# Kernel tuning notes

Measured on AMD Instinct MI355X. Metric: run time of the kernel, lower is better.

Reference implementation:

```python
import jax, jax.numpy as jnp
import numpy as np

N, E, DIN, DH, DOUT = 100000, 600000, 128, 128, 64


def _glorot(k, shape):
    lim = float(np.sqrt(6.0 / (shape[0] + shape[1])))
    return jax.random.uniform(k, shape, jnp.float32, -lim, lim)


def setup_inputs() -> dict:
    key = jax.random.key(0)
    ks = jax.random.split(key, 12)
    return {
        "x": jax.random.normal(ks[0], (N, DIN), jnp.float32),
        "src": jax.random.randint(ks[1], (E,), 0, N),
        "dst": jax.random.randint(ks[2], (E,), 0, N),
        # layer 0: NGNN_SAGEConv = SAGEConv(in,hid) + fc(hid,hid) + fc2(hid,hid)
        "w_self0": _glorot(ks[3], (DIN, DH)), "b_self0": jnp.zeros((DH,), jnp.float32),
        "w_neigh0": _glorot(ks[4], (DIN, DH)),
        "fc_w": _glorot(ks[5], (DH, DH)), "fc_b": jnp.zeros((DH,), jnp.float32),
        "fc2_w": _glorot(ks[6], (DH, DH)), "fc2_b": jnp.zeros((DH,), jnp.float32),
        # layer 1: SAGEConv(hid,hid)
        "w_self1": _glorot(ks[7], (DH, DH)), "b_self1": jnp.zeros((DH,), jnp.float32),
        "w_neigh1": _glorot(ks[8], (DH, DH)),
        # layer 2: SAGEConv(hid,out)
        "w_self2": _glorot(ks[9], (DH, DOUT)), "b_self2": jnp.zeros((DOUT,), jnp.float32),
        "w_neigh2": _glorot(ks[10], (DH, DOUT)),
    }


def _sage_conv(x, src, dst, w_self, b_self, w_neigh):
    # DGL SAGEConv, aggregator='mean': out = x @ W_self + b + mean_{u->v} x_u @ W_neigh
    agg = jax.ops.segment_sum(x[src], dst, num_segments=N)          # [N, d_in]
    deg = jax.ops.segment_sum(jnp.ones((src.shape[0],), x.dtype), dst, num_segments=N)
    h_neigh = agg / jnp.maximum(deg, 1.0)[:, None]                  # zero-in-degree -> 0
    return x @ w_self + b_self + h_neigh @ w_neigh


def reference(x, src, dst,
              w_self0, b_self0, w_neigh0, fc_w, fc_b, fc2_w, fc2_b,
              w_self1, b_self1, w_neigh1,
              w_self2, b_self2, w_neigh2):
    # layer 0: NGNN_SAGEConv with num_nonl_layers=2, then outer ReLU (dropout: eval = identity)
    h = _sage_conv(x, src, dst, w_self0, b_self0, w_neigh0)
    h = jax.nn.relu(h)
    h = h @ fc_w + fc_b
    h = jax.nn.relu(h)
    h = h @ fc2_w + fc2_b
    h = jax.nn.relu(h)
    # layer 1: SAGEConv + ReLU
    h = _sage_conv(h, src, dst, w_self1, b_self1, w_neigh1)
    h = jax.nn.relu(h)
    # layer 2 (output): SAGEConv, no activation
    return _sage_conv(h, src, dst, w_self2, b_self2, w_neigh2)
```

## Files before the change

kernel.cpp:

```cpp
#include <hip/hip_runtime.h>

#define N_NODES 100000
#define N_EDGES 600000
#define K_DIM   128
#define NPART   ((N_NODES + 255) / 256)
#define EBLK    ((N_EDGES + 255) / 256)
#define CASTB   (N_NODES * K_DIM / 8 / 256)

typedef unsigned short ushort_t;
typedef short v8s __attribute__((ext_vector_type(8)));
typedef float v4f __attribute__((ext_vector_type(4)));

__device__ __forceinline__ ushort_t f2b(float f) {
  unsigned u = __builtin_bit_cast(unsigned, f);
  unsigned r = u + 0x7FFFu + ((u >> 16) & 1u);
  return (ushort_t)(r >> 16);
}
__device__ __forceinline__ float b2f(ushort_t h) {
  return __builtin_bit_cast(float, (unsigned)h << 16);
}
__device__ __forceinline__ float blo(unsigned u) {
  return __builtin_bit_cast(float, u << 16);
}
__device__ __forceinline__ float bhi(unsigned u) {
  return __builtin_bit_cast(float, u & 0xFFFF0000u);
}


__global__ void deg_cast_kernel(const int* __restrict__ dst, int* __restrict__ deg,
                                const float* __restrict__ X, ushort_t* __restrict__ Xb) {
  if (blockIdx.x < EBLK) {
    int e = blockIdx.x * 256 + threadIdx.x;
    if (e < N_EDGES) atomicAdd(&deg[dst[e]], 1);
  } else {
    int i = ((blockIdx.x - EBLK) * 256 + threadIdx.x) * 8;
    if (i >= N_NODES * K_DIM) return;
    float4 v0 = *(const float4*)(X + i);
    float4 v1 = *(const float4*)(X + i + 4);
    ushort4 h0, h1;
    h0.x = f2b(v0.x); h0.y = f2b(v0.y); h0.z = f2b(v0.z); h0.w = f2b(v0.w);
    h1.x = f2b(v1.x); h1.y = f2b(v1.y); h1.z = f2b(v1.z); h1.w = f2b(v1.w);
    *(ushort4*)(Xb + i)     = h0;
    *(ushort4*)(Xb + i + 4) = h1;
  }
}

__global__ void scan1_swz_kernel(
    const int* __restrict__ deg, int* __restrict__ excl, int* __restrict__ partials,
    const float* __restrict__ w0, const float* __restrict__ w1,
    const float* __restrict__ w2, const float* __restrict__ w3,
    const float* __restrict__ w4, const float* __restrict__ w5,
    const float* __restrict__ w6, const float* __restrict__ w7,
    ushort_t* __restrict__ s0, ushort_t* __restrict__ s1,
    ushort_t* __restrict__ s2, ushort_t* __restrict__ s3,
    ushort_t* __restrict__ s4, ushort_t* __restrict__ s5,
    ushort_t* __restrict__ s6, ushort_t* __restrict__ s7) {
  __shared__ int s[256];
  if (blockIdx.x < NPART) {
    int t = threadIdx.x, i = blockIdx.x * 256 + t;
    int v = (i < N_NODES) ? deg[i] : 0;
    s[t] = v;
    __syncthreads();
    for (int off = 1; off < 256; off <<= 1) {
      int x = (t >= off) ? s[t - off] : 0;
      __syncthreads();
      s[t] += x;
      __syncthreads();
    }
    if (i < N_NODES) excl[i] = s[t] - v;
    if (t == 255) partials[blockIdx.x] = s[t];
  } else {
    const int blk = blockIdx.x - NPART;
    const int z = blk >> 6;
    const float* W;
    ushort_t* S;
    int dout = 128;
    switch (z) {
      case 0: W = w0; S = s0; break;
      case 1: W = w1; S = s1; break;
      case 2: W = w2; S = s2; break;
      case 3: W = w3; S = s3; break;
      case 4: W = w4; S = s4; break;
      case 5: W = w5; S = s5; break;
      case 6: W = w6; S = s6; dout = 64; break;
      default: W = w7; S = s7; dout = 64; break;
    }
    int t = (blk & 63) * 256 + threadIdx.x;
    if (t >= K_DIM * dout) return;
    int k = t / dout, n = t % dout;
    S[(k >> 3) * (dout * 8) + n * 8 + (k & 7)] = f2b(W[t]);
  }
}

__global__ void scan2_kernel(int* __restrict__ partials) {
  __shared__ int s[512];
  int t = threadIdx.x;
  int v = (t < NPART) ? partials[t] : 0;
  s[t] = v;
  __syncthreads();
  for (int off = 1; off < 512; off <<= 1) {
    int x = (t >= off) ? s[t - off] : 0;
    __syncthreads();
    s[t] += x;
    __syncthreads();
  }
  if (t < NPART) partials[t] = s[t] - v;
}

__global__ void scan3_kernel(const int* __restrict__ excl, const int* __restrict__ partials,
                             const int* __restrict__ deg, int* __restrict__ row_ptr,
                             int* __restrict__ cursor, float* __restrict__ inv_deg) {
  int i = blockIdx.x * blockDim.x + threadIdx.x;
  if (i < N_NODES) {
    int rp = excl[i] + partials[i >> 8];
    row_ptr[i] = rp;
    cursor[i] = rp;
    inv_deg[i] = 1.0f / (float)(deg[i] > 1 ? deg[i] : 1);
  } else if (i == N_NODES) {
    row_ptr[N_NODES] = N_EDGES;
  }
}

__global__ void fill_kernel(const int* __restrict__ src, const int* __restrict__ dst,
                            int* __restrict__ cursor, int* __restrict__ ssrc) {
  int e = blockIdx.x * blockDim.x + threadIdx.x;
  if (e < N_EDGES) {
    int p = atomicAdd(&cursor[dst[e]], 1);
    ssrc[p] = src[e];
  }
}


__global__ __launch_bounds__(256, 8) void agg_kernel(
    const ushort_t* __restrict__ Hh,
    const int* __restrict__ row_ptr, const int* __restrict__ ssrc,
    const float* __restrict__ inv_deg, ushort_t* __restrict__ Ah) {
  const int tid = threadIdx.x;
  const int c0  = (tid & 15) * 8;
  const int r   = tid >> 4;
  const int v   = blockIdx.x * 16 + r;
  if (v >= N_NODES) return;

  float a[8];
  #pragma unroll
  for (int i = 0; i < 8; ++i) a[i] = 0.f;

  const int beg = row_ptr[v], end = row_ptr[v + 1];
  int e = beg;
  for (; e + 4 <= end; e += 4) {
    const int s0 = ssrc[e];
    const int s1 = ssrc[e + 1];
    const int s2 = ssrc[e + 2];
    const int s3 = ssrc[e + 3];
    const uint4 p0 = *(const uint4*)(Hh + (size_t)s0 * K_DIM + c0);
    const uint4 p1 = *(const uint4*)(Hh + (size_t)s1 * K_DIM + c0);
    const uint4 p2 = *(const uint4*)(Hh + (size_t)s2 * K_DIM + c0);
    const uint4 p3 = *(const uint4*)(Hh + (size_t)s3 * K_DIM + c0);
    a[0] += (blo(p0.x) + blo(p1.x)) + (blo(p2.x) + blo(p3.x));
    a[1] += (bhi(p0.x) + bhi(p1.x)) + (bhi(p2.x) + bhi(p3.x));
    a[2] += (blo(p0.y) + blo(p1.y)) + (blo(p2.y) + blo(p3.y));
    a[3] += (bhi(p0.y) + bhi(p1.y)) + (bhi(p2.y) + bhi(p3.y));
    a[4] += (blo(p0.z) + blo(p1.z)) + (blo(p2.z) + blo(p3.z));
    a[5] += (bhi(p0.z) + bhi(p1.z)) + (bhi(p2.z) + bhi(p3.z));
    a[6] += (blo(p0.w) + blo(p1.w)) + (blo(p2.w) + blo(p3.w));
    a[7] += (bhi(p0.w) + bhi(p1.w)) + (bhi(p2.w) + bhi(p3.w));
  }
  if (e + 2 <= end) {
    const int s0 = ssrc[e];
    const int s1 = ssrc[e + 1];
    const uint4 p0 = *(const uint4*)(Hh + (size_t)s0 * K_DIM + c0);
    const uint4 p1 = *(const uint4*)(Hh + (size_t)s1 * K_DIM + c0);
    a[0] += blo(p0.x) + blo(p1.x);
    a[1] += bhi(p0.x) + bhi(p1.x);
    a[2] += blo(p0.y) + blo(p1.y);
    a[3] += bhi(p0.y) + bhi(p1.y);
    a[4] += blo(p0.z) + blo(p1.z);
    a[5] += bhi(p0.z) + bhi(p1.z);
    a[6] += blo(p0.w) + blo(p1.w);
    a[7] += bhi(p0.w) + bhi(p1.w);
    e += 2;
  }
  if (e < end) {
    const int s0 = ssrc[e];
    const uint4 p0 = *(const uint4*)(Hh + (size_t)s0 * K_DIM + c0);
    a[0] += blo(p0.x);
    a[1] += bhi(p0.x);
    a[2] += blo(p0.y);
    a[3] += bhi(p0.y);
    a[4] += blo(p0.z);
    a[5] += bhi(p0.z);
    a[6] += blo(p0.w);
    a[7] += bhi(p0.w);
  }
  const float sc = inv_deg[v];
  ushort4 o0, o1;
  o0.x = f2b(a[0] * sc); o0.y = f2b(a[1] * sc);
  o0.z = f2b(a[2] * sc); o0.w = f2b(a[3] * sc);
  o1.x = f2b(a[4] * sc); o1.y = f2b(a[5] * sc);
  o1.z = f2b(a[6] * sc); o1.w = f2b(a[7] * sc);
  const size_t wo = (size_t)v * K_DIM + c0;
  *(ushort4*)(Ah + wo)     = o0;
  *(ushort4*)(Ah + wo + 4) = o1;
}


template <int DOUT, bool RELU, bool BF16_OUT>
__global__ __launch_bounds__(512, 4) void mfma_gemm_kernel(
    const ushort_t* __restrict__ A1, const ushort_t* __restrict__ A2,
    const ushort_t* __restrict__ W1sw, const ushort_t* __restrict__ W2sw,
    const float* __restrict__ bias,
    ushort_t* __restrict__ Obf, float* __restrict__ Ofp) {
  constexpr int NT  = DOUT / 16;
  constexpr int SWN = K_DIM * DOUT;
  constexpr int NW  = SWN / 4096;
  __shared__ ushort_t bufW[SWN];

  const int tid   = threadIdx.x;
  const int wv    = tid >> 6;
  const int lane  = tid & 63;
  const int lm    = lane & 15;
  const int q     = lane >> 4;
  const int row0  = blockIdx.x * 128 + wv * 16;

  #pragma unroll
  for (int j = 0; j < NW; ++j)
    *(uint4*)&bufW[tid * 8 + j * 4096] = *(const uint4*)&W1sw[tid * 8 + j * 4096];
  uint4 wreg[NW];
  #pragma unroll
  for (int j = 0; j < NW; ++j)
    wreg[j] = *(const uint4*)&W2sw[tid * 8 + j * 4096];
  __syncthreads();

  int ra = row0 + lm;  ra = ra < N_NODES ? ra : N_NODES - 1;
  const size_t off0 = (size_t)ra * K_DIM;

  v4f acc[NT];
  #pragma unroll
  for (int n = 0; n < NT; ++n) acc[n] = (v4f){0.f, 0.f, 0.f, 0.f};

  for (int ks = 0; ks < K_DIM / 32; ++ks) {
    const int ko = ks * 32 + q * 8;
    const v8s a0 = *(const v8s*)(A1 + off0 + ko);
    #pragma unroll
    for (int nt = 0; nt < NT; ++nt) {
      const v8s b = *(const v8s*)&bufW[((ks * 4 + q) * DOUT + nt * 16 + lm) * 8];
      acc[nt] = __builtin_amdgcn_mfma_f32_16x16x32_bf16(a0, b, acc[nt], 0, 0, 0);
    }
  }
  __syncthreads();

  #pragma unroll
  for (int j = 0; j < NW; ++j)
    *(uint4*)&bufW[tid * 8 + j * 4096] = wreg[j];
  __syncthreads();

  for (int ks = 0; ks < K_DIM / 32; ++ks) {
    const int ko = ks * 32 + q * 8;
    const v8s a0 = *(const v8s*)(A2 + off0 + ko);
    #pragma unroll
    for (int nt = 0; nt < NT; ++nt) {
      const v8s b = *(const v8s*)&bufW[((ks * 4 + q) * DOUT + nt * 16 + lm) * 8];
      acc[nt] = __builtin_amdgcn_mfma_f32_16x16x32_bf16(a0, b, acc[nt], 0, 0, 0);
    }
  }

  #pragma unroll
  for (int nt = 0; nt < NT; ++nt) {
    const int col = nt * 16 + lm;
    const float bv = bias[col];
    #pragma unroll
    for (int r = 0; r < 4; ++r) {
      const int row = row0 + q * 4 + r;
      if (row < N_NODES) {
        float v = acc[nt][r] + bv;
        if (RELU) v = v > 0.f ? v : 0.f;
        if (BF16_OUT) Obf[(size_t)row * DOUT + col] = f2b(v);
        else          Ofp[(size_t)row * DOUT + col] = v;
      }
    }
  }
}


__global__ __launch_bounds__(512, 4) void fused_fc_kernel(
    const ushort_t* __restrict__ A,
    const ushort_t* __restrict__ W1sw, const ushort_t* __restrict__ W2sw,
    const float* __restrict__ b1, const float* __restrict__ b2,
    ushort_t* __restrict__ O) {
  constexpr int NT = 8;
  constexpr int HP = 136;
  __shared__ ushort_t bufW[K_DIM * 128];
  __shared__ ushort_t bufH[128 * HP];

  const int tid   = threadIdx.x;
  const int wv    = tid >> 6;
  const int lane  = tid & 63;
  const int lm    = lane & 15;
  const int q     = lane >> 4;
  const int lrow0 = wv * 16;
  const int row0  = blockIdx.x * 128 + lrow0;

  for (int i = tid * 8; i < K_DIM * 128; i += 4096)
    *(uint4*)&bufW[i] = *(const uint4*)&W1sw[i];

  uint4 wreg[4];
  #pragma unroll
  for (int j = 0; j < 4; ++j)
    wreg[j] = *(const uint4*)&W2sw[tid * 8 + j * 4096];

  __syncthreads();

  int ra = row0 + lm;  ra = ra < N_NODES ? ra : N_NODES - 1;
  const size_t off0 = (size_t)ra * K_DIM;

  v4f acc[NT];
  #pragma unroll
  for (int n = 0; n < NT; ++n) acc[n] = (v4f){0.f, 0.f, 0.f, 0.f};

  for (int ks = 0; ks < K_DIM / 32; ++ks) {
    const int ko = ks * 32 + q * 8;
    const v8s a0 = *(const v8s*)(A + off0 + ko);
    #pragma unroll
    for (int nt = 0; nt < NT; ++nt) {
      const v8s b = *(const v8s*)&bufW[((ks * 4 + q) * 128 + nt * 16 + lm) * 8];
      acc[nt] = __builtin_amdgcn_mfma_f32_16x16x32_bf16(a0, b, acc[nt], 0, 0, 0);
    }
  }
  __syncthreads();

  #pragma unroll
  for (int j = 0; j < 4; ++j)
    *(uint4*)&bufW[tid * 8 + j * 4096] = wreg[j];
  #pragma unroll
  for (int nt = 0; nt < NT; ++nt) {
    const int col = nt * 16 + lm;
    const float bv = b1[col];
    #pragma unroll
    for (int r = 0; r < 4; ++r) {
      float v = acc[nt][r] + bv;
      v = v > 0.f ? v : 0.f;
      bufH[(lrow0 + q * 4 + r) * HP + col] = f2b(v);
      acc[nt][r] = 0.f;
    }
  }
  __syncthreads();

  for (int ks = 0; ks < K_DIM / 32; ++ks) {
    const int ko = ks * 32 + q * 8;
    const v8s a0 = *(const v8s*)&bufH[(lrow0 + lm) * HP + ko];
    #pragma unroll
    for (int nt = 0; nt < NT; ++nt) {
      const v8s b = *(const v8s*)&bufW[((ks * 4 + q) * 128 + nt * 16 + lm) * 8];
      acc[nt] = __builtin_amdgcn_mfma_f32_16x16x32_bf16(a0, b, acc[nt], 0, 0, 0);
    }
  }

  #pragma unroll
  for (int nt = 0; nt < NT; ++nt) {
    const int col = nt * 16 + lm;
    const float bv = b2[col];
    #pragma unroll
    for (int r = 0; r < 4; ++r) {
      const int row = row0 + q * 4 + r;
      if (row < N_NODES) {
        float v = acc[nt][r] + bv;
        v = v > 0.f ? v : 0.f;
        O[(size_t)row * 128 + col] = f2b(v);
      }
    }
  }
}


extern "C" void kernel_launch(void* const* d_in, const int* in_sizes, int n_in,
                              void* d_out, int out_size, void* d_ws, size_t ws_size,
                              hipStream_t stream) {
  const float* x        = (const float*)d_in[0];
  const int*   src      = (const int*)d_in[1];
  const int*   dst      = (const int*)d_in[2];
  const float* w_self0  = (const float*)d_in[3];
  const float* b_self0  = (const float*)d_in[4];
  const float* w_neigh0 = (const float*)d_in[5];
  const float* fc_w     = (const float*)d_in[6];
  const float* fc_b     = (const float*)d_in[7];
  const float* fc2_w    = (const float*)d_in[8];
  const float* fc2_b    = (const float*)d_in[9];
  const float* w_self1  = (const float*)d_in[10];
  const float* b_self1  = (const float*)d_in[11];
  const float* w_neigh1 = (const float*)d_in[12];
  const float* w_self2  = (const float*)d_in[13];
  const float* b_self2  = (const float*)d_in[14];
  const float* w_neigh2 = (const float*)d_in[15];

  char* p = (char*)d_ws;
  auto carve = [&](size_t bytes) {
    void* q = (void*)p;
    p += (bytes + 511) & ~(size_t)511;
    return q;
  };
  const size_t PLANE = (size_t)N_NODES * K_DIM * sizeof(ushort_t);
  ushort_t* X   = (ushort_t*)carve(PLANE);
  ushort_t* Y   = (ushort_t*)carve(PLANE);
  ushort_t* Z   = (ushort_t*)carve(PLANE);
  ushort_t* ws0 = (ushort_t*)carve(K_DIM * 128 * 2);
  ushort_t* wn0 = (ushort_t*)carve(K_DIM * 128 * 2);
  ushort_t* wfc = (ushort_t*)carve(K_DIM * 128 * 2);
  ushort_t* wf2 = (ushort_t*)carve(K_DIM * 128 * 2);
  ushort_t* ws1 = (ushort_t*)carve(K_DIM * 128 * 2);
  ushort_t* wn1 = (ushort_t*)carve(K_DIM * 128 * 2);
  ushort_t* ws2 = (ushort_t*)carve(K_DIM * 64 * 2);
  ushort_t* wn2 = (ushort_t*)carve(K_DIM * 64 * 2);
  int*   ssrc    = (int*)carve((size_t)N_EDGES * 4);
  int*   row_ptr = (int*)carve((size_t)(N_NODES + 1) * 4);
  int*   cursor  = (int*)carve((size_t)N_NODES * 4);
  int*   deg     = (int*)carve((size_t)N_NODES * 4);
  int*   excl    = (int*)carve((size_t)N_NODES * 4);
  int*   parts   = (int*)carve(512 * 4);
  float* inv_deg = (float*)carve((size_t)N_NODES * 4);

  hipMemsetAsync(deg, 0, (size_t)N_NODES * 4, stream);
  deg_cast_kernel<<<EBLK + CASTB, 256, 0, stream>>>(dst, deg, x, X);
  scan1_swz_kernel<<<NPART + 512, 256, 0, stream>>>(
      deg, excl, parts,
      w_self0, w_neigh0, fc_w, fc2_w, w_self1, w_neigh1, w_self2, w_neigh2,
      ws0, wn0, wfc, wf2, ws1, wn1, ws2, wn2);
  scan2_kernel<<<1, 512, 0, stream>>>(parts);
  scan3_kernel<<<((N_NODES + 1) + 255) / 256, 256, 0, stream>>>(excl, parts, deg,
                                                                row_ptr, cursor, inv_deg);
  fill_kernel<<<EBLK, 256, 0, stream>>>(src, dst, cursor, ssrc);

  const int AB = (N_NODES + 15) / 16;
  const int GB = (N_NODES + 127) / 128;

  agg_kernel<<<AB, 256, 0, stream>>>(X, row_ptr, ssrc, inv_deg, Y);
  mfma_gemm_kernel<128, true, true><<<GB, 512, 0, stream>>>(
      X, Y, ws0, wn0, b_self0, Z, nullptr);
  fused_fc_kernel<<<GB, 512, 0, stream>>>(Z, wfc, wf2, fc_b, fc2_b, Y);
  agg_kernel<<<AB, 256, 0, stream>>>(Y, row_ptr, ssrc, inv_deg, X);
  mfma_gemm_kernel<128, true, true><<<GB, 512, 0, stream>>>(
      Y, X, ws1, wn1, b_self1, Z, nullptr);
  agg_kernel<<<AB, 256, 0, stream>>>(Z, row_ptr, ssrc, inv_deg, Y);
  mfma_gemm_kernel<64, false, false><<<GB, 512, 0, stream>>>(
      Z, Y, ws2, wn2, b_self2, nullptr, (float*)d_out);
}
```

Before: 392.4 us.

## Fuse neighbor mean aggregation into SAGE GEMM kernel via shared-memory staging

Merges the separate aggregation kernel into the MFMA GEMM kernel. Each block gathers and averages neighbor features for its 128 rows into a padded LDS tile, then reads that tile as the A operand of the neighbor GEMM. This removes the global write and re-read of the aggregated bf16 matrix and three kernel launches per forward. In exchange, LDS use per block grows by about 34 KB, which may lower occupancy, and the gather now runs inside a 512-thread block with fewer independent gather streams per thread.

```diff
diff --git a/kernel.cpp b/kernel.cpp
--- a/kernel.cpp
+++ b/kernel.cpp
@@ -24,6 +24,9 @@
 }
 __device__ __forceinline__ float bhi(unsigned u) {
   return __builtin_bit_cast(float, u & 0xFFFF0000u);
+}
+__device__ __forceinline__ unsigned pk2(float lo, float hi) {
+  return (unsigned)f2b(lo) | ((unsigned)f2b(hi) << 16);
 }
 
 
@@ -131,105 +134,103 @@
 }
 
 
-__global__ __launch_bounds__(256, 8) void agg_kernel(
-    const ushort_t* __restrict__ Hh,
+template <int DOUT, bool RELU, bool BF16_OUT>
+__global__ __launch_bounds__(512, 4) void sage_layer_kernel(
+    const ushort_t* __restrict__ H,
+    const ushort_t* __restrict__ Wself_sw, const ushort_t* __restrict__ Wneigh_sw,
+    const float* __restrict__ bias,
     const int* __restrict__ row_ptr, const int* __restrict__ ssrc,
-    const float* __restrict__ inv_deg, ushort_t* __restrict__ Ah) {
-  const int tid = threadIdx.x;
-  const int c0  = (tid & 15) * 8;
-  const int r   = tid >> 4;
-  const int v   = blockIdx.x * 16 + r;
-  if (v >= N_NODES) return;
-
-  float a[8];
-  #pragma unroll
-  for (int i = 0; i < 8; ++i) a[i] = 0.f;
-
-  const int beg = row_ptr[v], end = row_ptr[v + 1];
-  int e = beg;
-  for (; e + 4 <= end; e += 4) {
-    const int s0 = ssrc[e];
-    const int s1 = ssrc[e + 1];
-    const int s2 = ssrc[e + 2];
-    const int s3 = ssrc[e + 3];
-    const uint4 p0 = *(const uint4*)(Hh + (size_t)s0 * K_DIM + c0);
-    const uint4 p1 = *(const uint4*)(Hh + (size_t)s1 * K_DIM + c0);
-    const uint4 p2 = *(const uint4*)(Hh + (size_t)s2 * K_DIM + c0);
-    const uint4 p3 = *(const uint4*)(Hh + (size_t)s3 * K_DIM + c0);
-    a[0] += (blo(p0.x) + blo(p1.x)) + (blo(p2.x) + blo(p3.x));
-    a[1] += (bhi(p0.x) + bhi(p1.x)) + (bhi(p2.x) + bhi(p3.x));
-    a[2] += (blo(p0.y) + blo(p1.y)) + (blo(p2.y) + blo(p3.y));
-    a[3] += (bhi(p0.y) + bhi(p1.y)) + (bhi(p2.y) + bhi(p3.y));
-    a[4] += (blo(p0.z) + blo(p1.z)) + (blo(p2.z) + blo(p3.z));
-    a[5] += (bhi(p0.z) + bhi(p1.z)) + (bhi(p2.z) + bhi(p3.z));
-    a[6] += (blo(p0.w) + blo(p1.w)) + (blo(p2.w) + blo(p3.w));
-    a[7] += (bhi(p0.w) + bhi(p1.w)) + (bhi(p2.w) + bhi(p3.w));
-  }
-  if (e + 2 <= end) {
-    const int s0 = ssrc[e];
-    const int s1 = ssrc[e + 1];
-    const uint4 p0 = *(const uint4*)(Hh + (size_t)s0 * K_DIM + c0);
-    const uint4 p1 = *(const uint4*)(Hh + (size_t)s1 * K_DIM + c0);
-    a[0] += blo(p0.x) + blo(p1.x);
-    a[1] += bhi(p0.x) + bhi(p1.x);
-    a[2] += blo(p0.y) + blo(p1.y);
-    a[3] += bhi(p0.y) + bhi(p1.y);
-    a[4] += blo(p0.z) + blo(p1.z);
-    a[5] += bhi(p0.z) + bhi(p1.z);
-    a[6] += blo(p0.w) + blo(p1.w);
-    a[7] += bhi(p0.w) + bhi(p1.w);
-    e += 2;
-  }
-  if (e < end) {
-    const int s0 = ssrc[e];
-    const uint4 p0 = *(const uint4*)(Hh + (size_t)s0 * K_DIM + c0);
-    a[0] += blo(p0.x);
-    a[1] += bhi(p0.x);
-    a[2] += blo(p0.y);
-    a[3] += bhi(p0.y);
-    a[4] += blo(p0.z);
-    a[5] += bhi(p0.z);
-    a[6] += blo(p0.w);
-    a[7] += bhi(p0.w);
-  }
-  const float sc = inv_deg[v];
-  ushort4 o0, o1;
-  o0.x = f2b(a[0] * sc); o0.y = f2b(a[1] * sc);
-  o0.z = f2b(a[2] * sc); o0.w = f2b(a[3] * sc);
-  o1.x = f2b(a[4] * sc); o1.y = f2b(a[5] * sc);
-  o1.z = f2b(a[6] * sc); o1.w = f2b(a[7] * sc);
-  const size_t wo = (size_t)v * K_DIM + c0;
-  *(ushort4*)(Ah + wo)     = o0;
-  *(ushort4*)(Ah + wo + 4) = o1;
-}
-
-
-template <int DOUT, bool RELU, bool BF16_OUT>
-__global__ __launch_bounds__(512, 4) void mfma_gemm_kernel(
-    const ushort_t* __restrict__ A1, const ushort_t* __restrict__ A2,
-    const ushort_t* __restrict__ W1sw, const ushort_t* __restrict__ W2sw,
-    const float* __restrict__ bias,
+    const float* __restrict__ inv_deg,
     ushort_t* __restrict__ Obf, float* __restrict__ Ofp) {
   constexpr int NT  = DOUT / 16;
   constexpr int SWN = K_DIM * DOUT;
   constexpr int NW  = SWN / 4096;
+  constexpr int HP  = 136;
   __shared__ ushort_t bufW[SWN];
+  __shared__ ushort_t aggb[128 * HP];
 
   const int tid   = threadIdx.x;
   const int wv    = tid >> 6;
   const int lane  = tid & 63;
   const int lm    = lane & 15;
   const int q     = lane >> 4;
-  const int row0  = blockIdx.x * 128 + wv * 16;
+  const int lrow0 = wv * 16;
+  const int row0  = blockIdx.x * 128 + lrow0;
 
   #pragma unroll
   for (int j = 0; j < NW; ++j)
-    *(uint4*)&bufW[tid * 8 + j * 4096] = *(const uint4*)&W1sw[tid * 8 + j * 4096];
+    *(uint4*)&bufW[tid * 8 + j * 4096] = *(const uint4*)&Wself_sw[tid * 8 + j * 4096];
   uint4 wreg[NW];
   #pragma unroll
   for (int j = 0; j < NW; ++j)
-    wreg[j] = *(const uint4*)&W2sw[tid * 8 + j * 4096];
-  __syncthreads();
+    wreg[j] = *(const uint4*)&Wneigh_sw[tid * 8 + j * 4096];
+  __syncthreads();
+
+  {
+    const int c0 = lm * 8;
+    for (int rr = 0; rr < 4; ++rr) {
+      const int lr = q * 4 + rr;
+      int gv = row0 + lr;
+      const int vv = gv < N_NODES ? gv : N_NODES - 1;
+      float a[8];
+      #pragma unroll
+      for (int i = 0; i < 8; ++i) a[i] = 0.f;
+      const int beg = row_ptr[vv], end = row_ptr[vv + 1];
+      int e = beg;
+      for (; e + 4 <= end; e += 4) {
+        const int s0 = ssrc[e];
+        const int s1 = ssrc[e + 1];
+        const int s2 = ssrc[e + 2];
+        const int s3 = ssrc[e + 3];
+        const uint4 p0 = *(const uint4*)(H + (size_t)s0 * K_DIM + c0);
+        const uint4 p1 = *(const uint4*)(H + (size_t)s1 * K_DIM + c0);
+        const uint4 p2 = *(const uint4*)(H + (size_t)s2 * K_DIM + c0);
+        const uint4 p3 = *(const uint4*)(H + (size_t)s3 * K_DIM + c0);
+        a[0] += (blo(p0.x) + blo(p1.x)) + (blo(p2.x) + blo(p3.x));
+        a[1] += (bhi(p0.x) + bhi(p1.x)) + (bhi(p2.x) + bhi(p3.x));
+        a[2] += (blo(p0.y) + blo(p1.y)) + (blo(p2.y) + blo(p3.y));
+        a[3] += (bhi(p0.y) + bhi(p1.y)) + (bhi(p2.y) + bhi(p3.y));
+        a[4] += (blo(p0.z) + blo(p1.z)) + (blo(p2.z) + blo(p3.z));
+        a[5] += (bhi(p0.z) + bhi(p1.z)) + (bhi(p2.z) + bhi(p3.z));
+        a[6] += (blo(p0.w) + blo(p1.w)) + (blo(p2.w) + blo(p3.w));
+        a[7] += (bhi(p0.w) + bhi(p1.w)) + (bhi(p2.w) + bhi(p3.w));
+      }
+      if (e + 2 <= end) {
+        const int s0 = ssrc[e];
+        const int s1 = ssrc[e + 1];
+        const uint4 p0 = *(const uint4*)(H + (size_t)s0 * K_DIM + c0);
+        const uint4 p1 = *(const uint4*)(H + (size_t)s1 * K_DIM + c0);
+        a[0] += blo(p0.x) + blo(p1.x);
+        a[1] += bhi(p0.x) + bhi(p1.x);
+        a[2] += blo(p0.y) + blo(p1.y);
+        a[3] += bhi(p0.y) + bhi(p1.y);
+        a[4] += blo(p0.z) + blo(p1.z);
+        a[5] += bhi(p0.z) + bhi(p1.z);
+        a[6] += blo(p0.w) + blo(p1.w);
+        a[7] += bhi(p0.w) + bhi(p1.w);
+        e += 2;
+      }
+      if (e < end) {
+        const int s0 = ssrc[e];
+        const uint4 p0 = *(const uint4*)(H + (size_t)s0 * K_DIM + c0);
+        a[0] += blo(p0.x);
+        a[1] += bhi(p0.x);
+        a[2] += blo(p0.y);
+        a[3] += bhi(p0.y);
+        a[4] += blo(p0.z);
+        a[5] += bhi(p0.z);
+        a[6] += blo(p0.w);
+        a[7] += bhi(p0.w);
+      }
+      const float sc = inv_deg[vv];
+      uint4 ov;
+      ov.x = pk2(a[0] * sc, a[1] * sc);
+      ov.y = pk2(a[2] * sc, a[3] * sc);
+      ov.z = pk2(a[4] * sc, a[5] * sc);
+      ov.w = pk2(a[6] * sc, a[7] * sc);
+      *(uint4*)&aggb[(lrow0 + lr) * HP + c0] = ov;
+    }
+  }
 
   int ra = row0 + lm;  ra = ra < N_NODES ? ra : N_NODES - 1;
   const size_t off0 = (size_t)ra * K_DIM;
@@ -240,7 +241,7 @@
 
   for (int ks = 0; ks < K_DIM / 32; ++ks) {
     const int ko = ks * 32 + q * 8;
-    const v8s a0 = *(const v8s*)(A1 + off0 + ko);
+    const v8s a0 = *(const v8s*)(H + off0 + ko);
     #pragma unroll
     for (int nt = 0; nt < NT; ++nt) {
       const v8s b = *(const v8s*)&bufW[((ks * 4 + q) * DOUT + nt * 16 + lm) * 8];
@@ -256,7 +257,7 @@
 
   for (int ks = 0; ks < K_DIM / 32; ++ks) {
     const int ko = ks * 32 + q * 8;
-    const v8s a0 = *(const v8s*)(A2 + off0 + ko);
+    const v8s a0 = *(const v8s*)&aggb[(lrow0 + lm) * HP + ko];
     #pragma unroll
     for (int nt = 0; nt < NT; ++nt) {
       const v8s b = *(const v8s*)&bufW[((ks * 4 + q) * DOUT + nt * 16 + lm) * 8];
@@ -429,17 +430,13 @@
                                                                 row_ptr, cursor, inv_deg);
   fill_kernel<<<EBLK, 256, 0, stream>>>(src, dst, cursor, ssrc);
 
-  const int AB = (N_NODES + 15) / 16;
   const int GB = (N_NODES + 127) / 128;
 
-  agg_kernel<<<AB, 256, 0, stream>>>(X, row_ptr, ssrc, inv_deg, Y);
-  mfma_gemm_kernel<128, true, true><<<GB, 512, 0, stream>>>(
-      X, Y, ws0, wn0, b_self0, Z, nullptr);
+  sage_layer_kernel<128, true, true><<<GB, 512, 0, stream>>>(
+      X, ws0, wn0, b_self0, row_ptr, ssrc, inv_deg, Z, nullptr);
   fused_fc_kernel<<<GB, 512, 0, stream>>>(Z, wfc, wf2, fc_b, fc2_b, Y);
-  agg_kernel<<<AB, 256, 0, stream>>>(Y, row_ptr, ssrc, inv_deg, X);
-  mfma_gemm_kernel<128, true, true><<<GB, 512, 0, stream>>>(
-      Y, X, ws1, wn1, b_self1, Z, nullptr);
-  agg_kernel<<<AB, 256, 0, stream>>>(Z, row_ptr, ssrc, inv_deg, Y);
-  mfma_gemm_kernel<64, false, false><<<GB, 512, 0, stream>>>(
-      Z, Y, ws2, wn2, b_self2, nullptr, (float*)d_out);
-}
+  sage_layer_kernel<128, true, true><<<GB, 512, 0, stream>>>(
+      Y, ws1, wn1, b_self1, row_ptr, ssrc, inv_deg, Z, nullptr);
+  sage_layer_kernel<64, false, false><<<GB, 512, 0, stream>>>(
+      Z, ws2, wn2, b_self2, row_ptr, ssrc, inv_deg, nullptr, (float*)d_out);
+}
```

After: 379.1 us. -3.4%, faster.
